# Optimization experiments

Hardware: AMD Instinct MI355X
Metric: run time of the kernel (lower is better)

The kernel has to match this reference:

```python
import jax, jax.numpy as jnp
import numpy as np

B, S, N = 8, 64, 256
STATE, IN_F, OUT_F = 128, 64, 64
ALPHA = 0.2
NEG = -9e15


def setup_inputs() -> dict:
    key = jax.random.key(0)
    ks = jax.random.split(key, 12)
    d = {
        "hyper_inputs": jax.random.normal(ks[0], (B, S, STATE), jnp.float32),
        "inputs": jax.random.normal(ks[1], (B, S, N, IN_F), jnp.float32),
        "Adj": jax.random.randint(ks[2], (N, N), 0, 2, jnp.int32),
        # hyper_w: Linear(STATE,32) -> ReLU -> Linear(32, OUT_F*IN_F)
        "w1": jax.random.normal(ks[3], (STATE, 32), jnp.float32) * 0.08,
        "b1": jax.random.normal(ks[4], (32,), jnp.float32) * 0.01,
        "w2": jax.random.normal(ks[5], (32, OUT_F * IN_F), jnp.float32) * 0.08,
        "b2": jax.random.normal(ks[6], (OUT_F * IN_F,), jnp.float32) * 0.01,
        # hyper_a: Linear(STATE,32) -> ReLU -> Linear(32, 2*OUT_F)
        "aw1": jax.random.normal(ks[7], (STATE, 32), jnp.float32) * 0.08,
        "ab1": jax.random.normal(ks[8], (32,), jnp.float32) * 0.01,
        "aw2": jax.random.normal(ks[9], (32, 2 * OUT_F), jnp.float32) * 0.08,
        "ab2": jax.random.normal(ks[10], (2 * OUT_F,), jnp.float32) * 0.01,
    }
    return d


def _leaky(x):
    return jnp.where(x >= 0, x, ALPHA * x)


def reference(hyper_inputs, inputs, Adj, w1, b1, w2, b2, aw1, ab1, aw2, ab2):
    # hypernetwork-generated per-(b,s) weights
    hdn = jax.nn.relu(hyper_inputs @ w1 + b1)            # [B,S,32]
    W = jnp.abs(hdn @ w2 + b2).reshape(B, S, IN_F, OUT_F)
    hda = jax.nn.relu(hyper_inputs @ aw1 + ab1)
    a = jnp.abs(hda @ aw2 + ab2)                          # [B,S,2*OUT_F]

    h = jnp.einsum('bsni,bsio->bsno', inputs, W)          # [B,S,N,OUT_F]

    # decomposed GAT scores: e[b,s,i,j] = leakyrelu(h_i.a1 + h_j.a2)
    a1, a2 = a[..., :OUT_F], a[..., OUT_F:]
    e1 = jnp.einsum('bsno,bso->bsn', h, a1)               # source term
    e2 = jnp.einsum('bsno,bso->bsn', h, a2)               # target term
    e = _leaky(e1[..., :, None] + e2[..., None, :])       # [B,S,N,N]

    attention = jnp.where(Adj > 0, e, NEG)
    # NOTE: faithful to original: softmax over dim=1 (the S axis)
    attention = jax.nn.softmax(attention, axis=1)
    h_prime = jnp.einsum('bsij,bsjo->bsio', attention, h)  # [B,S,N,OUT_F]
    return jax.nn.elu(h_prime)                              # concat=True branch
```

## Files before the change

kernel.cpp:

```cpp
#include <hip/hip_runtime.h>
#include <hip/hip_bf16.h>
#include <math.h>

#define BB 8
#define SS 64
#define NN 256
#define ST 128
#define IF 64
#define OF 64
#define H1 32
#define ALPHA 0.2f
#define LOG2E 1.4426950408889634f

typedef short short8 __attribute__((ext_vector_type(8)));
typedef short short4_t __attribute__((ext_vector_type(4)));
typedef float f32x4 __attribute__((ext_vector_type(4)));
typedef unsigned short ushort_t;

static __device__ __forceinline__ ushort_t f2bf(float f) {
    __hip_bfloat16 h = __float2bfloat16(f);
    return *reinterpret_cast<ushort_t*>(&h);
}

__global__ __launch_bounds__(512) void k_hyper2(
    const float* __restrict__ hyper,
    const float* __restrict__ w1, const float* __restrict__ b1,
    const float* __restrict__ w2, const float* __restrict__ b2,
    const float* __restrict__ aw1, const float* __restrict__ ab1,
    const float* __restrict__ aw2, const float* __restrict__ ab2,
    float* __restrict__ Wd, float* __restrict__ Aa)
{
    const int t = threadIdx.x;
    const int bs0 = blockIdx.x * 2;
    __shared__ float hy[2][ST];
    __shared__ float hdn_s[2][H1];
    __shared__ float hda_s[2][H1];
    if (t < 2 * ST)
        hy[t >> 7][t & 127] = hyper[(size_t)bs0 * ST + t];
    __syncthreads();
    if (t < 64) {
        const int q = t >> 5, c = t & 31;
        float acc = b1[c];
#pragma unroll 4
        for (int k = 0; k < ST; ++k) acc = fmaf(hy[q][k], w1[k * H1 + c], acc);
        hdn_s[q][c] = fmaxf(acc, 0.f);
    } else if (t < 128) {
        const int tt = t - 64;
        const int q = tt >> 5, c = tt & 31;
        float acc = ab1[c];
#pragma unroll 4
        for (int k = 0; k < ST; ++k) acc = fmaf(hy[q][k], aw1[k * H1 + c], acc);
        hda_s[q][c] = fmaxf(acc, 0.f);
    }
    __syncthreads();
    if (t < 256) {
        const int q = t >> 7, c = t & 127;
        float a = ab2[c];
#pragma unroll
        for (int k = 0; k < H1; ++k)
            a = fmaf(hda_s[q][k], aw2[k * 128 + c], a);
        Aa[(size_t)(bs0 + q) * 128 + c] = fabsf(a);
    }
#pragma unroll
    for (int p = 0; p < 2; ++p) {
        const int e = t * 4 + p * 2048;
        const float4 bb = *(const float4*)&b2[e];
        float4 a0 = bb, a1 = bb;
#pragma unroll
        for (int kq = 0; kq < 8; ++kq) {
            const float4 h0 = *(const float4*)&hdn_s[0][kq * 4];
            const float4 h1 = *(const float4*)&hdn_s[1][kq * 4];
#pragma unroll
            for (int c = 0; c < 4; ++c) {
                const float4 wv = *(const float4*)&w2[(size_t)(kq * 4 + c) * 4096 + e];
                const float s0 = (c == 0) ? h0.x : (c == 1) ? h0.y : (c == 2) ? h0.z : h0.w;
                const float s1 = (c == 0) ? h1.x : (c == 1) ? h1.y : (c == 2) ? h1.z : h1.w;
                a0.x = fmaf(s0, wv.x, a0.x); a0.y = fmaf(s0, wv.y, a0.y);
                a0.z = fmaf(s0, wv.z, a0.z); a0.w = fmaf(s0, wv.w, a0.w);
                a1.x = fmaf(s1, wv.x, a1.x); a1.y = fmaf(s1, wv.y, a1.y);
                a1.z = fmaf(s1, wv.z, a1.z); a1.w = fmaf(s1, wv.w, a1.w);
            }
        }
        a0.x = fabsf(a0.x); a0.y = fabsf(a0.y); a0.z = fabsf(a0.z); a0.w = fabsf(a0.w);
        a1.x = fabsf(a1.x); a1.y = fabsf(a1.y); a1.z = fabsf(a1.z); a1.w = fabsf(a1.w);
        *(float4*)&Wd[(size_t)(bs0 + 0) * 4096 + e] = a0;
        *(float4*)&Wd[(size_t)(bs0 + 1) * 4096 + e] = a1;
    }
}

__global__ __launch_bounds__(256) void k_h(
    const float* __restrict__ x, const float* __restrict__ Wd,
    const float* __restrict__ Aa,
    ushort_t* __restrict__ HbTw, float* __restrict__ E1, float* __restrict__ E2)
{
    const int bs = blockIdx.x;
    const int tid = threadIdx.x;
    const int wid = tid >> 6;
    const int lane = tid & 63;
    const int l15 = lane & 15;
    const int lhi = lane >> 4;

    __shared__ char xl[NN * IF * 4];
    __shared__ ushort_t Wt[IF * OF];
    __shared__ float wa1s[IF], wa2s[IF];
    __shared__ float a1s[OF], a2s[OF];

    if (tid < 64) a1s[tid] = Aa[(size_t)bs * 128 + tid];
    else if (tid < 128) a2s[tid - 64] = Aa[(size_t)bs * 128 + tid];

    {
        const float4* x4 = (const float4*)(x + (size_t)bs * NN * IF);
#pragma unroll
        for (int p = 0; p < 16; ++p) {
            const int idx = tid + p * 256;
            const int row = idx >> 4;
            const int byte = (row << 8) | ((((idx & 15) << 4)) ^ ((row & 7) << 5));
            *(float4*)(xl + byte) = x4[idx];
        }
    }
    {
        const float4* w4 = (const float4*)(Wd + (size_t)bs * 4096);
#pragma unroll
        for (int p = 0; p < 4; ++p) {
            const int idx = tid + p * 256;
            const float4 f = w4[idx];
            const int k = (idx * 4) >> 6;
            const int o0 = (idx * 4) & 63;
            Wt[(o0 + 0) * 64 + (k ^ (((o0 + 0) & 7) << 3))] = f2bf(f.x);
            Wt[(o0 + 1) * 64 + (k ^ (((o0 + 1) & 7) << 3))] = f2bf(f.y);
            Wt[(o0 + 2) * 64 + (k ^ (((o0 + 2) & 7) << 3))] = f2bf(f.z);
            Wt[(o0 + 3) * 64 + (k ^ (((o0 + 3) & 7) << 3))] = f2bf(f.w);
        }
    }
    __syncthreads();

    if (tid < 64) {
        const float4* wr = (const float4*)(Wd + (size_t)bs * 4096 + tid * 64);
        float s1 = 0.f, s2 = 0.f;
#pragma unroll
        for (int q = 0; q < 16; ++q) {
            const float4 f = wr[q];
            const float4 u = *(const float4*)&a1s[q * 4];
            const float4 v = *(const float4*)&a2s[q * 4];
            s1 += f.x * u.x + f.y * u.y + f.z * u.z + f.w * u.w;
            s2 += f.x * v.x + f.y * v.y + f.z * v.z + f.w * v.w;
        }
        wa1s[tid] = s1; wa2s[tid] = s2;
    }
    __syncthreads();

    {
        float s1 = 0.f, s2 = 0.f;
        const int rbase = tid << 8;
        const int sw = (tid & 7) << 5;
#pragma unroll
        for (int q = 0; q < 16; ++q) {
            const float4 f = *(const float4*)(xl + (rbase | ((q << 4) ^ sw)));
            const float4 u = *(const float4*)&wa1s[q * 4];
            const float4 v = *(const float4*)&wa2s[q * 4];
            s1 += f.x * u.x + f.y * u.y + f.z * u.z + f.w * u.w;
            s2 += f.x * v.x + f.y * v.y + f.z * v.z + f.w * v.w;
        }
        E1[(size_t)bs * NN + tid] = s1 * LOG2E;
        E2[(size_t)bs * NN + tid] = s2 * LOG2E;
    }

    f32x4 acc[4][4];
#pragma unroll
    for (int mt = 0; mt < 4; ++mt)
#pragma unroll
        for (int nt = 0; nt < 4; ++nt) acc[mt][nt] = (f32x4){0.f, 0.f, 0.f, 0.f};

    short8 af[4][2];
#pragma unroll
    for (int mt = 0; mt < 4; ++mt) {
        const int row = wid * 64 + mt * 16 + l15;
        const int rb = row << 8;
        const int sw = (row & 7) << 5;
#pragma unroll
        for (int ks = 0; ks < 2; ++ks) {
            const int kb = (ks * 32 + lhi * 8) * 4;
            const float4 fa = *(const float4*)(xl + (rb | (kb ^ sw)));
            const float4 fb = *(const float4*)(xl + (rb | ((kb + 16) ^ sw)));
            short8 pk;
            pk[0] = (short)f2bf(fa.x); pk[1] = (short)f2bf(fa.y);
            pk[2] = (short)f2bf(fa.z); pk[3] = (short)f2bf(fa.w);
            pk[4] = (short)f2bf(fb.x); pk[5] = (short)f2bf(fb.y);
            pk[6] = (short)f2bf(fb.z); pk[7] = (short)f2bf(fb.w);
            af[mt][ks] = pk;
        }
    }
    short8 bfr[4][2];
#pragma unroll
    for (int nt = 0; nt < 4; ++nt) {
        const int o = nt * 16 + l15;
#pragma unroll
        for (int ks = 0; ks < 2; ++ks) {
            const int k0 = ks * 32 + lhi * 8;
            bfr[nt][ks] = *(const short8*)&Wt[o * 64 + (k0 ^ ((o & 7) << 3))];
        }
    }
#pragma unroll
    for (int mt = 0; mt < 4; ++mt)
#pragma unroll
        for (int nt = 0; nt < 4; ++nt) {
            acc[mt][nt] = __builtin_amdgcn_mfma_f32_16x16x32_bf16(
                af[mt][0], bfr[nt][0], acc[mt][nt], 0, 0, 0);
            acc[mt][nt] = __builtin_amdgcn_mfma_f32_16x16x32_bf16(
                af[mt][1], bfr[nt][1], acc[mt][nt], 0, 0, 0);
        }

    ushort_t* hbw = HbTw + (size_t)bs * (OF * NN);
#pragma unroll
    for (int mt = 0; mt < 4; ++mt) {
        const int nb = wid * 8 + mt * 2 + (lhi >> 1);
        const int ne = (lhi & 1) * 4;
#pragma unroll
        for (int nt = 0; nt < 4; ++nt) {
            short4_t pk;
            pk[0] = (short)f2bf(acc[mt][nt][0]);
            pk[1] = (short)f2bf(acc[mt][nt][1]);
            pk[2] = (short)f2bf(acc[mt][nt][2]);
            pk[3] = (short)f2bf(acc[mt][nt][3]);
            *(short4_t*)(hbw + ((size_t)(nt * 32 + nb) * 16 + l15) * 8 + ne) = pk;
        }
    }
}

__global__ __launch_bounds__(256) void k_softstats(
    const float* __restrict__ E1, const float* __restrict__ E2,
    const int* __restrict__ Adj, unsigned int* __restrict__ MRw)
{
    const int b = blockIdx.x & 7;
    const int i0 = (blockIdx.x >> 3) * 4;
    const int t = threadIdx.x;
    __shared__ float e1s[4][SS];
    {
        const int ii = t >> 6, s = t & 63;
        e1s[ii][s] = E1[(size_t)(b * SS + s) * NN + i0 + ii];
    }
    float e2r[SS];
#pragma unroll
    for (int s = 0; s < SS; ++s)
        e2r[s] = E2[(size_t)(b * SS + s) * NN + t];
    __syncthreads();

#pragma unroll
    for (int ii = 0; ii < 4; ++ii) {
        float v[SS];
        float mx = -3.0e38f;
#pragma unroll
        for (int s = 0; s < SS; ++s) {
            float u = e1s[ii][s] + e2r[s];
            u = fmaxf(u, ALPHA * u);
            v[s] = u;
            mx = fmaxf(mx, u);
        }
        const unsigned int mu = (unsigned int)f2bf(mx);
        const float mUse = __uint_as_float(mu << 16);
        float sum = 0.f;
#pragma unroll
        for (int s = 0; s < SS; ++s)
            sum += exp2f(v[s] - mUse);
        const int i = i0 + ii;
        const int adj = Adj[(size_t)i * NN + t];
        const float r = (adj > 0) ? (1.f / sum) : -0.015625f;
        MRw[((((size_t)b * 16 + (i >> 4)) * 32 + (t >> 3)) * 16 + (i & 15)) * 8
            + (t & 7)] = (mu << 16) | (unsigned int)f2bf(r);
    }
}

__global__ __launch_bounds__(256, 4) void k_attn(
    const ushort_t* __restrict__ HbTw, const float* __restrict__ E1,
    const float* __restrict__ E2, const unsigned int* __restrict__ MRw,
    float* __restrict__ out)
{
    const int b = blockIdx.x & 7;
    const int k2 = blockIdx.x >> 3;
    const int s = k2 >> 1;
    const int half = k2 & 1;
    const int bs = b * 64 + s;
    const int tid = threadIdx.x;
    const int wid = tid >> 6;
    const int lane = tid & 63;
    const int l15 = lane & 15;
    const int lhi = lane >> 4;
    const int rb0 = half * 128 + wid * 32;

    __shared__ float e2s[NN];
    e2s[tid] = E2[(size_t)bs * NN + tid];
    __syncthreads();

    float e1r[2];
#pragma unroll
    for (int mt = 0; mt < 2; ++mt)
        e1r[mt] = E1[(size_t)bs * NN + rb0 + mt * 16 + l15];

    f32x4 acc[2][4];
#pragma unroll
    for (int mt = 0; mt < 2; ++mt)
#pragma unroll
        for (int nt = 0; nt < 4; ++nt) acc[mt][nt] = (f32x4){0.f, 0.f, 0.f, 0.f};

    const ushort_t* hbw = HbTw + (size_t)bs * (OF * NN);
    const unsigned int* mrb = MRw + (size_t)b * (NN * NN);
    const unsigned int* mr0 = mrb + ((size_t)((rb0 >> 4) + 0) * 32) * 128 + l15 * 8;
    const unsigned int* mr1 = mrb + ((size_t)((rb0 >> 4) + 1) * 32) * 128 + l15 * 8;

    for (int ch = 0; ch < 4; ++ch) {
#pragma unroll
        for (int ks = 0; ks < 2; ++ks) {
            const int kb = ch * 8 + ks * 4 + lhi;
            short8 bfr[4];
#pragma unroll
            for (int nt = 0; nt < 4; ++nt)
                bfr[nt] = *(const short8*)(hbw + ((size_t)(nt * 32 + kb) * 16 + l15) * 8);
            uint4 mq[2][2];
            mq[0][0] = *(const uint4*)(mr0 + kb * 128);
            mq[0][1] = *(const uint4*)(mr0 + kb * 128 + 4);
            mq[1][0] = *(const uint4*)(mr1 + kb * 128);
            mq[1][1] = *(const uint4*)(mr1 + kb * 128 + 4);
            const int k0 = ch * 64 + ks * 32 + lhi * 8;
            const float4 lo = *(const float4*)&e2s[k0];
            const float4 hi = *(const float4*)&e2s[k0 + 4];
            const float e2v[8] = {lo.x, lo.y, lo.z, lo.w, hi.x, hi.y, hi.z, hi.w};
#pragma unroll
            for (int mt = 0; mt < 2; ++mt) {
                const float e1v = e1r[mt];
                const unsigned int wv[8] = {
                    mq[mt][0].x, mq[mt][0].y, mq[mt][0].z, mq[mt][0].w,
                    mq[mt][1].x, mq[mt][1].y, mq[mt][1].z, mq[mt][1].w};
                short8 pk;
#pragma unroll
                for (int kk = 0; kk < 8; ++kk) {
                    const float Mf = __uint_as_float(wv[kk] & 0xFFFF0000u);
                    const float Rf = __uint_as_float(wv[kk] << 16);
                    float v = e1v + e2v[kk];
                    v = fmaxf(v, ALPHA * v);
                    const float a = (Rf < 0.f) ? -Rf : exp2f(v - Mf) * Rf;
                    pk[kk] = (short)f2bf(a);
                }
#pragma unroll
                for (int nt = 0; nt < 4; ++nt)
                    acc[mt][nt] = __builtin_amdgcn_mfma_f32_16x16x32_bf16(
                        pk, bfr[nt], acc[mt][nt], 0, 0, 0);
            }
        }
    }

    float* ob = out + (size_t)bs * (NN * OF);
#pragma unroll
    for (int mt = 0; mt < 2; ++mt) {
        const int rbase = rb0 + mt * 16 + lhi * 4;
#pragma unroll
        for (int nt = 0; nt < 4; ++nt) {
            const int o = nt * 16 + l15;
#pragma unroll
            for (int reg = 0; reg < 4; ++reg) {
                float v = acc[mt][nt][reg];
                v = (v > 0.f) ? v : (__expf(v) - 1.f);
                ob[(size_t)(rbase + reg) * OF + o] = v;
            }
        }
    }
}

extern "C" void kernel_launch(void* const* d_in, const int* in_sizes, int n_in,
                              void* d_out, int out_size, void* d_ws, size_t ws_size,
                              hipStream_t stream)
{
    const float* hyper = (const float*)d_in[0];
    const float* x     = (const float*)d_in[1];
    const int*   Adj   = (const int*)d_in[2];
    const float* w1    = (const float*)d_in[3];
    const float* b1    = (const float*)d_in[4];
    const float* w2    = (const float*)d_in[5];
    const float* b2    = (const float*)d_in[6];
    const float* aw1   = (const float*)d_in[7];
    const float* ab1   = (const float*)d_in[8];
    const float* aw2   = (const float*)d_in[9];
    const float* ab2   = (const float*)d_in[10];
    float* out = (float*)d_out;

    float* ws      = (float*)d_ws;
    float* Wd      = ws;
    float* Aa      = Wd + 2097152;
    ushort_t* HbTw = (ushort_t*)(Aa + 65536);
    float* E1      = (float*)(HbTw + 8388608);
    float* E2      = E1 + 131072;
    unsigned int* MRw = (unsigned int*)(E2 + 131072);

    k_hyper2<<<dim3(256), dim3(512), 0, stream>>>(hyper, w1, b1, w2, b2,
                                                  aw1, ab1, aw2, ab2, Wd, Aa);
    k_h<<<dim3(512), dim3(256), 0, stream>>>(x, Wd, Aa, HbTw, E1, E2);
    k_softstats<<<dim3(512), dim3(256), 0, stream>>>(E1, E2, Adj, MRw);
    k_attn<<<dim3(1024), dim3(256), 0, stream>>>(HbTw, E1, E2, MRw, out);
}
```

Before: 73.24 us.

## Retile attention kernel so each wave shares mask tile across two sequence steps

Each block of the attention kernel now handles two consecutive s values and a quarter of the rows, with each wave covering 16 rows for both s values instead of 32 rows for one s. The per-batch max/reciprocal mask tile (MRw), which does not depend on s, is loaded once and reused for both s, halving mask traffic. In exchange, the hidden-state B fragments are loaded for two s values per wave instead of one. Grid size and register usage stay roughly the same.

```diff
diff --git a/kernel.cpp b/kernel.cpp
--- a/kernel.cpp
+++ b/kernel.cpp
@@ -276,60 +276,61 @@
     float* __restrict__ out)
 {
     const int b = blockIdx.x & 7;
-    const int k2 = blockIdx.x >> 3;
-    const int s = k2 >> 1;
-    const int half = k2 & 1;
-    const int bs = b * 64 + s;
+    const int q = blockIdx.x >> 3;
+    const int s0 = (q >> 2) * 2;
+    const int quarter = q & 3;
+    const int bs0 = b * 64 + s0;
     const int tid = threadIdx.x;
     const int wid = tid >> 6;
     const int lane = tid & 63;
     const int l15 = lane & 15;
     const int lhi = lane >> 4;
-    const int rb0 = half * 128 + wid * 32;
-
-    __shared__ float e2s[NN];
-    e2s[tid] = E2[(size_t)bs * NN + tid];
+    const int rb0 = quarter * 64 + wid * 16;
+    const int rg = rb0 >> 4;
+
+    __shared__ float e2s[2][NN];
+    e2s[0][tid] = E2[(size_t)bs0 * NN + tid];
+    e2s[1][tid] = E2[(size_t)(bs0 + 1) * NN + tid];
     __syncthreads();
 
     float e1r[2];
-#pragma unroll
-    for (int mt = 0; mt < 2; ++mt)
-        e1r[mt] = E1[(size_t)bs * NN + rb0 + mt * 16 + l15];
+    e1r[0] = E1[(size_t)bs0 * NN + rb0 + l15];
+    e1r[1] = E1[(size_t)(bs0 + 1) * NN + rb0 + l15];
 
     f32x4 acc[2][4];
 #pragma unroll
-    for (int mt = 0; mt < 2; ++mt)
-#pragma unroll
-        for (int nt = 0; nt < 4; ++nt) acc[mt][nt] = (f32x4){0.f, 0.f, 0.f, 0.f};
-
-    const ushort_t* hbw = HbTw + (size_t)bs * (OF * NN);
-    const unsigned int* mrb = MRw + (size_t)b * (NN * NN);
-    const unsigned int* mr0 = mrb + ((size_t)((rb0 >> 4) + 0) * 32) * 128 + l15 * 8;
-    const unsigned int* mr1 = mrb + ((size_t)((rb0 >> 4) + 1) * 32) * 128 + l15 * 8;
+    for (int sp = 0; sp < 2; ++sp)
+#pragma unroll
+        for (int nt = 0; nt < 4; ++nt) acc[sp][nt] = (f32x4){0.f, 0.f, 0.f, 0.f};
+
+    const ushort_t* hbw0 = HbTw + (size_t)bs0 * (OF * NN);
+    const ushort_t* hbw1 = hbw0 + OF * NN;
+    const unsigned int* mr = MRw + (size_t)b * (NN * NN)
+                           + ((size_t)rg * 32) * 128 + l15 * 8;
 
     for (int ch = 0; ch < 4; ++ch) {
 #pragma unroll
         for (int ks = 0; ks < 2; ++ks) {
             const int kb = ch * 8 + ks * 4 + lhi;
-            short8 bfr[4];
-#pragma unroll
-            for (int nt = 0; nt < 4; ++nt)
-                bfr[nt] = *(const short8*)(hbw + ((size_t)(nt * 32 + kb) * 16 + l15) * 8);
-            uint4 mq[2][2];
-            mq[0][0] = *(const uint4*)(mr0 + kb * 128);
-            mq[0][1] = *(const uint4*)(mr0 + kb * 128 + 4);
-            mq[1][0] = *(const uint4*)(mr1 + kb * 128);
-            mq[1][1] = *(const uint4*)(mr1 + kb * 128 + 4);
+            short8 bfr[2][4];
+#pragma unroll
+            for (int nt = 0; nt < 4; ++nt) {
+                const size_t off = ((size_t)(nt * 32 + kb) * 16 + l15) * 8;
+                bfr[0][nt] = *(const short8*)(hbw0 + off);
+                bfr[1][nt] = *(const short8*)(hbw1 + off);
+            }
+            const uint4 m0 = *(const uint4*)(mr + kb * 128);
+            const uint4 m1 = *(const uint4*)(mr + kb * 128 + 4);
+            const unsigned int wv[8] = {m0.x, m0.y, m0.z, m0.w,
+                                        m1.x, m1.y, m1.z, m1.w};
             const int k0 = ch * 64 + ks * 32 + lhi * 8;
-            const float4 lo = *(const float4*)&e2s[k0];
-            const float4 hi = *(const float4*)&e2s[k0 + 4];
-            const float e2v[8] = {lo.x, lo.y, lo.z, lo.w, hi.x, hi.y, hi.z, hi.w};
-#pragma unroll
-            for (int mt = 0; mt < 2; ++mt) {
-                const float e1v = e1r[mt];
-                const unsigned int wv[8] = {
-                    mq[mt][0].x, mq[mt][0].y, mq[mt][0].z, mq[mt][0].w,
-                    mq[mt][1].x, mq[mt][1].y, mq[mt][1].z, mq[mt][1].w};
+#pragma unroll
+            for (int sp = 0; sp < 2; ++sp) {
+                const float4 lo = *(const float4*)&e2s[sp][k0];
+                const float4 hi = *(const float4*)&e2s[sp][k0 + 4];
+                const float e2v[8] = {lo.x, lo.y, lo.z, lo.w,
+                                      hi.x, hi.y, hi.z, hi.w};
+                const float e1v = e1r[sp];
                 short8 pk;
 #pragma unroll
                 for (int kk = 0; kk < 8; ++kk) {
@@ -342,22 +343,22 @@
                 }
 #pragma unroll
                 for (int nt = 0; nt < 4; ++nt)
-                    acc[mt][nt] = __builtin_amdgcn_mfma_f32_16x16x32_bf16(
-                        pk, bfr[nt], acc[mt][nt], 0, 0, 0);
+                    acc[sp][nt] = __builtin_amdgcn_mfma_f32_16x16x32_bf16(
+                        pk, bfr[sp][nt], acc[sp][nt], 0, 0, 0);
             }
         }
     }
 
-    float* ob = out + (size_t)bs * (NN * OF);
-#pragma unroll
-    for (int mt = 0; mt < 2; ++mt) {
-        const int rbase = rb0 + mt * 16 + lhi * 4;
+#pragma unroll
+    for (int sp = 0; sp < 2; ++sp) {
+        float* ob = out + (size_t)(bs0 + sp) * (NN * OF);
+        const int rbase = rb0 + lhi * 4;
 #pragma unroll
         for (int nt = 0; nt < 4; ++nt) {
             const int o = nt * 16 + l15;
 #pragma unroll
             for (int reg = 0; reg < 4; ++reg) {
-                float v = acc[mt][nt][reg];
+                float v = acc[sp][nt][reg];
                 v = (v > 0.f) ? v : (__expf(v) - 1.f);
                 ob[(size_t)(rbase + reg) * OF + o] = v;
             }
```

Result: slower. 76.81 us (+4.9%).
